# Optimization experiments

Hardware: AMD Instinct MI355X
Metric: run time of the kernel (lower is better)

## Reference

```python
import jax, jax.numpy as jnp
import numpy as np

B, H, T = 32, 80, 1600
C1, C2 = 32, 32
K, S, P = 3, 2, 1  # kernel, stride, padding on both dims


def setup_inputs() -> dict:
    key = jax.random.key(0)
    k1, k2, k3, k4, k5, k6 = jax.random.split(key, 6)
    inputs = jax.random.normal(k1, (B, 1, H, T), dtype=jnp.float32)
    seq_lengths = jax.random.randint(k2, (B,), 1, T + 1).astype(jnp.int32)
    W1 = jax.random.normal(k3, (C1, 1, K, K), dtype=jnp.float32) * 0.1
    b1 = jax.random.normal(k4, (C1,), dtype=jnp.float32) * 0.1
    W2 = jax.random.normal(k5, (C2, C1, K, K), dtype=jnp.float32) * 0.05
    b2 = jax.random.normal(k6, (C2,), dtype=jnp.float32) * 0.1
    return {"inputs": inputs, "seq_lengths": seq_lengths,
            "W1": W1, "b1": b1, "W2": W2, "b2": b2}


def _conv(x, W, b):
    y = jax.lax.conv_general_dilated(
        x, W, window_strides=(S, S), padding=((P, P), (P, P)),
        dimension_numbers=("NCHW", "OIHW", "NCHW"))
    return y + b[None, :, None, None]


def _new_lengths(L):
    # floor((L + 2p - d*(k-1) - 1)/s) + 1, matching _get_sequence_lengths
    return (L + 2 * P - (K - 1) - 1) // S + 1


def _mask_time(x, L):
    # zero positions t >= L[b] along the last (time) axis
    t = jnp.arange(x.shape[3])
    valid = (t[None, :] < L[:, None]).astype(x.dtype)  # [B, Tout]
    return x * valid[:, None, None, :]


def reference(inputs, seq_lengths, W1, b1, W2, b2):
    # conv1 + mask
    x = _conv(inputs, W1, b1)
    L = _new_lengths(seq_lengths)
    x = _mask_time(x, L)
    # relu + mask (lengths unchanged)
    x = _mask_time(jax.nn.relu(x), L)
    # conv2 + mask
    x = _conv(x, W2, b2)
    L = _new_lengths(L)
    x = _mask_time(x, L)
    # relu + mask
    x = _mask_time(jax.nn.relu(x), L)
    return x, L
```

## Files before the change

kernel.cpp:

```cpp
#include <hip/hip_runtime.h>
#include <hip/hip_bf16.h>

#define B_    32
#define H_IN  80
#define T_IN  1600
#define C1_   32
#define H1_   40
#define T1_   800
#define C2_   32
#define H2_   20
#define T2_   400

#define TH2   2
#define TT2   32
#define NH1   5
#define NT1   65
#define NIDX  33
#define RROWS 11
#define RCOLSW 66
#define RWORDS (RROWS * RCOLSW)

#define NPOS   (NH1 * NT1)
#define NCHUNK 11

#define WS_W2FRAGS 1152
#define WS_W1OFF   1152
#define WS_TOTAL   1216
#define OUTN  (B_ * C2_ * H2_ * T2_)

typedef unsigned int uint32;
typedef __attribute__((ext_vector_type(8)))  short short8;
typedef __attribute__((ext_vector_type(4)))  float f32x4;
typedef __attribute__((ext_vector_type(16))) float f32x16;
typedef __attribute__((ext_vector_type(2)))  uint32 u32x2;
typedef __attribute__((ext_vector_type(4)))  uint32 u32x4;

__device__ __forceinline__ unsigned short f2bf(float x) {
    __hip_bfloat16 h = __float2bfloat16(x);
    return __builtin_bit_cast(unsigned short, h);
}

__device__ __forceinline__ int x1off(int h1r, int t1r, int g) {
    int idx = t1r >> 1;
    int par = t1r & 1;
    return ((par * (NH1 * NIDX) + h1r * NIDX + idx) << 6) + (((g ^ idx) & 3) << 4);
}

__global__ void wprep(const float* __restrict__ W2, const float* __restrict__ W1,
                      const float* __restrict__ b1, unsigned short* __restrict__ ws) {
    int i = blockIdx.x * 256 + threadIdx.x;
    if (i < WS_W2FRAGS) {
        int mt   = i / 576;
        int rem  = i - mt * 576;
        int tap  = rem >> 6;
        int lane = rem & 63;
        int lg   = lane >> 4;
        int l15  = lane & 15;
        int c2   = mt * 16 + l15;
        short8 f;
#pragma unroll
        for (int j = 0; j < 8; ++j)
            f[j] = (short)f2bf(W2[((c2 * C1_) + lg * 8 + j) * 9 + tap]);
        *((short8*)ws + i) = f;
    } else if (i < WS_TOTAL) {
        int lane = i - WS_W1OFF;
        int c1 = lane & 31;
        int kb = (lane >> 5) * 8;
        short8 f;
#pragma unroll
        for (int j = 0; j < 8; ++j) {
            int k = kb + j;
            float v = (k < 9) ? W1[c1 * 9 + k] : (k == 9 ? b1[c1] : 0.0f);
            f[j] = (short)f2bf(v);
        }
        *((short8*)ws + i) = f;
    }
}

__global__ __launch_bounds__(256, 6) void fused_conv(
    const float* __restrict__ in, const int* __restrict__ seq,
    const float* __restrict__ b2,
    const unsigned short* __restrict__ ws,
    float* __restrict__ out)
{
    __shared__ __align__(16) char   x1mem[2 * NH1 * NIDX * 64];
    __shared__ __align__(16) uint32 raw32[RWORDS];

    const int tid  = threadIdx.x;
    const int lane = tid & 63;
    const int wv   = tid >> 6;
    const int l15  = lane & 15;
    const int lg   = lane >> 4;
    const int hi   = lane >> 5;
    const int n32  = lane & 31;
    const int b      = blockIdx.z;
    const int h2base = blockIdx.y * TH2;
    const int t2base = blockIdx.x * TT2;

    const int L  = seq[b];
    const int L1 = ((L  - 1) >> 1) + 1;
    const int L2 = ((L1 - 1) >> 1) + 1;

    if (blockIdx.x == 0 && blockIdx.y == 0 && tid == 0)
        out[OUTN + b] = (float)L2;

    if (t2base >= L2) {
#pragma unroll
        for (int k = 0; k < 8; ++k) {
            int i = tid + k * 256;
            int row = i >> 5, col = i & 31;
            int c2 = row >> 1, r = row & 1;
            int t2 = t2base + col;
            if (t2 < T2_)
                out[((b * C2_ + c2) * H2_ + h2base + r) * T2_ + t2] = 0.0f;
        }
        return;
    }

    const int row0 = 4 * h2base - 3;
    const int t0   = 4 * t2base - 3;
    const float* inb = in + b * (H_IN * T_IN);
#pragma unroll
    for (int k = 0; k < 3; ++k) {
        int pi = tid + k * 256;
        if (pi < RWORDS) {
            int row = pi / RCOLSW;
            int q   = pi - row * RCOLSW;
            int h = row0 + row;
            int t = t0 + 2 * q;
            bool hok = (h >= 0) & (h < H_IN);
            bool ok0 = hok & (t >= 0) & (t < T_IN);
            bool ok1 = hok & (t + 1 >= 0) & (t + 1 < T_IN);
            float v0 = inb[ok0 ? h * T_IN + t     : 0];
            float v1 = inb[ok1 ? h * T_IN + t + 1 : 0];
            v0 = ok0 ? v0 : 0.0f;
            v1 = ok1 ? v1 : 0.0f;
            raw32[pi] = (uint32)f2bf(v0) | ((uint32)f2bf(v1) << 16);
        }
    }

    const short8 w1f = *((const short8*)ws + WS_W1OFF + lane);
    const int mt    = wv & 1;
    const int strip = wv >> 1;
    short8 afr[9];
#pragma unroll
    for (int tap = 0; tap < 9; ++tap)
        afr[tap] = *((const short8*)ws + (mt * 9 + tap) * 64 + lane);
    float b2r[4];
#pragma unroll
    for (int j = 0; j < 4; ++j) b2r[j] = b2[mt * 16 + lg * 4 + j];

    __syncthreads();

    const int h1base = 2 * h2base - 1;
    const int t1base = 2 * t2base - 1;
    for (int c = wv; c < NCHUNK; c += 4) {
        int p  = c * 32 + n32;
        int pc = p < NPOS ? p : NPOS - 1;
        int h1r = pc / NT1;
        int t1r = pc - h1r * NT1;

        const uint32* rp = raw32 + (2 * h1r) * RCOLSW + t1r;
        uint32 a0 = rp[0],            b0v = rp[1];
        uint32 a1 = rp[RCOLSW],       b1v = rp[RCOLSW + 1];
        uint32 a2 = rp[2 * RCOLSW],   b2v = rp[2 * RCOLSW + 1];

        uint32 w0l = a0;
        uint32 w1l = (b0v & 0xffffu) | (a1 << 16);
        uint32 w2l = (a1 >> 16) | (b1v << 16);
        uint32 w3l = a2;
        uint32 w0h = (b2v & 0xffffu) | 0x3f800000u;

        uint32 fw0 = hi ? w0h : w0l;
        uint32 fw1 = hi ? 0u  : w1l;
        uint32 fw2 = hi ? 0u  : w2l;
        uint32 fw3 = hi ? 0u  : w3l;
        short8 bfrag = __builtin_bit_cast(short8, (u32x4){fw0, fw1, fw2, fw3});

        f32x16 acc = {};
        acc = __builtin_amdgcn_mfma_f32_32x32x16_bf16(w1f, bfrag, acc, 0, 0, 0);

        int h1 = h1base + h1r;
        int t1 = t1base + t1r;
        bool okp = (h1 >= 0) && (t1 >= 0) && (t1 < L1);
        if (p < NPOS) {
#pragma unroll
            for (int g = 0; g < 4; ++g) {
                float v0 = okp ? fmaxf(acc[4 * g + 0], 0.0f) : 0.0f;
                float v1 = okp ? fmaxf(acc[4 * g + 1], 0.0f) : 0.0f;
                float v2 = okp ? fmaxf(acc[4 * g + 2], 0.0f) : 0.0f;
                float v3 = okp ? fmaxf(acc[4 * g + 3], 0.0f) : 0.0f;
                u32x2 dw;
                dw.x = (uint32)f2bf(v0) | ((uint32)f2bf(v1) << 16);
                dw.y = (uint32)f2bf(v2) | ((uint32)f2bf(v3) << 16);
                *(u32x2*)(x1mem + x1off(h1r, t1r, g) + hi * 8) = dw;
            }
        }
    }

    __syncthreads();

    f32x4 acc2[TH2];
#pragma unroll
    for (int r = 0; r < TH2; ++r) acc2[r] = (f32x4){0.f, 0.f, 0.f, 0.f};

#pragma unroll
    for (int tap = 0; tap < 9; ++tap) {
        const int kh = tap / 3;
        const int kt = tap % 3;
        const int t1r = 2 * (strip * 16 + l15) + kt;
#pragma unroll
        for (int r = 0; r < TH2; ++r) {
            short8 bx = *(const short8*)(x1mem + x1off(2 * r + kh, t1r, lg));
            acc2[r] = __builtin_amdgcn_mfma_f32_16x16x32_bf16(afr[tap], bx, acc2[r], 0, 0, 0);
        }
    }

    __syncthreads();

    float* obuf = (float*)x1mem;
    {
        const int t2 = t2base + strip * 16 + l15;
        const bool vm = (t2 < L2);
#pragma unroll
        for (int r = 0; r < TH2; ++r) {
#pragma unroll
            for (int j = 0; j < 4; ++j) {
                int c2 = mt * 16 + lg * 4 + j;
                float v = acc2[r][j] + b2r[j];
                v = vm ? fmaxf(v, 0.0f) : 0.0f;
                obuf[(c2 * TH2 + r) * 33 + strip * 16 + l15] = v;
            }
        }
    }
    __syncthreads();

#pragma unroll
    for (int k = 0; k < 8; ++k) {
        int i = tid + k * 256;
        int row = i >> 5, col = i & 31;
        int c2 = row >> 1, r = row & 1;
        int t2 = t2base + col;
        if (t2 < T2_)
            out[((b * C2_ + c2) * H2_ + h2base + r) * T2_ + t2] = obuf[row * 33 + col];
    }
}

extern "C" void kernel_launch(void* const* d_in, const int* in_sizes, int n_in,
                              void* d_out, int out_size, void* d_ws, size_t ws_size,
                              hipStream_t stream) {
    const float* in  = (const float*)d_in[0];
    const int*   seq = (const int*)d_in[1];
    const float* W1  = (const float*)d_in[2];
    const float* b1  = (const float*)d_in[3];
    const float* W2  = (const float*)d_in[4];
    const float* b2  = (const float*)d_in[5];
    float* out = (float*)d_out;
    unsigned short* ws = (unsigned short*)d_ws;

    wprep<<<dim3((WS_TOTAL + 255) / 256), dim3(256), 0, stream>>>(W2, W1, b1, ws);

    dim3 grid((T2_ + TT2 - 1) / TT2, H2_ / TH2, B_);
    fused_conv<<<grid, dim3(256), 0, stream>>>(in, seq, b2, ws, out);
}
```

Before: 26.59 us.

## Double h2 tile height and switch conv2 to 32x32 MFMA with direct stores

Measured after the change: 26.97 us. No clear change (+1.4%).

```diff
diff --git a/kernel.cpp b/kernel.cpp
--- a/kernel.cpp
+++ b/kernel.cpp
@@ -11,17 +11,17 @@
 #define H2_   20
 #define T2_   400
 
-#define TH2   2
+#define TH2   4
 #define TT2   32
-#define NH1   5
+#define NH1   9
 #define NT1   65
 #define NIDX  33
-#define RROWS 11
+#define RROWS 19
 #define RCOLSW 66
 #define RWORDS (RROWS * RCOLSW)
 
 #define NPOS   (NH1 * NT1)
-#define NCHUNK 11
+#define NCHUNK 19
 
 #define WS_W2FRAGS 1152
 #define WS_W1OFF   1152
@@ -50,17 +50,16 @@
                       const float* __restrict__ b1, unsigned short* __restrict__ ws) {
     int i = blockIdx.x * 256 + threadIdx.x;
     if (i < WS_W2FRAGS) {
-        int mt   = i / 576;
-        int rem  = i - mt * 576;
-        int tap  = rem >> 6;
-        int lane = rem & 63;
-        int lg   = lane >> 4;
-        int l15  = lane & 15;
-        int c2   = mt * 16 + l15;
+        int th   = i >> 6;
+        int lane = i & 63;
+        int tap  = th >> 1;
+        int half = th & 1;
+        int c2   = lane & 31;
+        int hi   = lane >> 5;
         short8 f;
 #pragma unroll
         for (int j = 0; j < 8; ++j)
-            f[j] = (short)f2bf(W2[((c2 * C1_) + lg * 8 + j) * 9 + tap]);
+            f[j] = (short)f2bf(W2[(c2 * C1_ + half * 16 + hi * 8 + j) * 9 + tap]);
         *((short8*)ws + i) = f;
     } else if (i < WS_TOTAL) {
         int lane = i - WS_W1OFF;
@@ -77,7 +76,7 @@
     }
 }
 
-__global__ __launch_bounds__(256, 6) void fused_conv(
+__global__ __launch_bounds__(256, 3) void fused_conv(
     const float* __restrict__ in, const int* __restrict__ seq,
     const float* __restrict__ b2,
     const unsigned short* __restrict__ ws,
@@ -89,8 +88,6 @@
     const int tid  = threadIdx.x;
     const int lane = tid & 63;
     const int wv   = tid >> 6;
-    const int l15  = lane & 15;
-    const int lg   = lane >> 4;
     const int hi   = lane >> 5;
     const int n32  = lane & 31;
     const int b      = blockIdx.z;
@@ -105,14 +102,15 @@
         out[OUTN + b] = (float)L2;
 
     if (t2base >= L2) {
-#pragma unroll
-        for (int k = 0; k < 8; ++k) {
+        const f32x4 z4 = (f32x4){0.f, 0.f, 0.f, 0.f};
+#pragma unroll
+        for (int k = 0; k < 4; ++k) {
             int i = tid + k * 256;
-            int row = i >> 5, col = i & 31;
-            int c2 = row >> 1, r = row & 1;
-            int t2 = t2base + col;
-            if (t2 < T2_)
-                out[((b * C2_ + c2) * H2_ + h2base + r) * T2_ + t2] = 0.0f;
+            int row = i >> 3, colq = i & 7;
+            int c2 = row >> 2, r = row & 3;
+            int t2q = t2base + colq * 4;
+            if (t2q < T2_)
+                *(f32x4*)(out + ((b * C2_ + c2) * H2_ + h2base + r) * T2_ + t2q) = z4;
         }
         return;
     }
@@ -121,7 +119,7 @@
     const int t0   = 4 * t2base - 3;
     const float* inb = in + b * (H_IN * T_IN);
 #pragma unroll
-    for (int k = 0; k < 3; ++k) {
+    for (int k = 0; k < 5; ++k) {
         int pi = tid + k * 256;
         if (pi < RWORDS) {
             int row = pi / RCOLSW;
@@ -140,15 +138,12 @@
     }
 
     const short8 w1f = *((const short8*)ws + WS_W1OFF + lane);
-    const int mt    = wv & 1;
-    const int strip = wv >> 1;
-    short8 afr[9];
-#pragma unroll
-    for (int tap = 0; tap < 9; ++tap)
-        afr[tap] = *((const short8*)ws + (mt * 9 + tap) * 64 + lane);
-    float b2r[4];
-#pragma unroll
-    for (int j = 0; j < 4; ++j) b2r[j] = b2[mt * 16 + lg * 4 + j];
+    f32x4 b2v4[4];
+    {
+        const f32x4* b2p = (const f32x4*)b2;
+#pragma unroll
+        for (int q = 0; q < 4; ++q) b2v4[q] = b2p[2 * q + hi];
+    }
 
     __syncthreads();
 
@@ -200,49 +195,32 @@
 
     __syncthreads();
 
-    f32x4 acc2[TH2];
-#pragma unroll
-    for (int r = 0; r < TH2; ++r) acc2[r] = (f32x4){0.f, 0.f, 0.f, 0.f};
-
+    const int r = wv;
+    f32x16 acc = {};
 #pragma unroll
     for (int tap = 0; tap < 9; ++tap) {
         const int kh = tap / 3;
         const int kt = tap % 3;
-        const int t1r = 2 * (strip * 16 + l15) + kt;
-#pragma unroll
-        for (int r = 0; r < TH2; ++r) {
-            short8 bx = *(const short8*)(x1mem + x1off(2 * r + kh, t1r, lg));
-            acc2[r] = __builtin_amdgcn_mfma_f32_16x16x32_bf16(afr[tap], bx, acc2[r], 0, 0, 0);
-        }
-    }
-
-    __syncthreads();
-
-    float* obuf = (float*)x1mem;
-    {
-        const int t2 = t2base + strip * 16 + l15;
+        const int t1r = 2 * n32 + kt;
+#pragma unroll
+        for (int half = 0; half < 2; ++half) {
+            short8 a = *((const short8*)ws + (tap * 2 + half) * 64 + lane);
+            short8 bx = *(const short8*)(x1mem + x1off(2 * r + kh, t1r, half * 2 + hi));
+            acc = __builtin_amdgcn_mfma_f32_32x32x16_bf16(a, bx, acc, 0, 0, 0);
+        }
+    }
+
+    const int t2 = t2base + n32;
+    if (t2 < T2_) {
         const bool vm = (t2 < L2);
-#pragma unroll
-        for (int r = 0; r < TH2; ++r) {
-#pragma unroll
-            for (int j = 0; j < 4; ++j) {
-                int c2 = mt * 16 + lg * 4 + j;
-                float v = acc2[r][j] + b2r[j];
-                v = vm ? fmaxf(v, 0.0f) : 0.0f;
-                obuf[(c2 * TH2 + r) * 33 + strip * 16 + l15] = v;
-            }
-        }
-    }
-    __syncthreads();
-
-#pragma unroll
-    for (int k = 0; k < 8; ++k) {
-        int i = tid + k * 256;
-        int row = i >> 5, col = i & 31;
-        int c2 = row >> 1, r = row & 1;
-        int t2 = t2base + col;
-        if (t2 < T2_)
-            out[((b * C2_ + c2) * H2_ + h2base + r) * T2_ + t2] = obuf[row * 33 + col];
+        float* outb = out + ((b * C2_) * H2_ + h2base + r) * T2_ + t2;
+#pragma unroll
+        for (int reg = 0; reg < 16; ++reg) {
+            int c2 = (reg & 3) + 8 * (reg >> 2) + 4 * hi;
+            float v = acc[reg] + b2v4[reg >> 2][reg & 3];
+            v = vm ? fmaxf(v, 0.0f) : 0.0f;
+            outb[c2 * (H2_ * T2_)] = v;
+        }
     }
 }
 
```

## Convert fused conv to persistent blocks with register-prefetched input tiles

Applied to the files above, without the earlier changes.

Result: slower. 38.76 us (+45.8%).

```diff
diff --git a/kernel.cpp b/kernel.cpp
--- a/kernel.cpp
+++ b/kernel.cpp
@@ -23,6 +23,10 @@
 #define NPOS   (NH1 * NT1)
 #define NCHUNK 11
 
+#define NQ      130
+#define NBLK    1280
+#define QSTRIDE (NBLK / B_)
+
 #define WS_W2FRAGS 1152
 #define WS_W1OFF   1152
 #define WS_TOTAL   1216
@@ -44,6 +48,32 @@
     int idx = t1r >> 1;
     int par = t1r & 1;
     return ((par * (NH1 * NIDX) + h1r * NIDX + idx) << 6) + (((g ^ idx) & 3) << 4);
+}
+
+__device__ __forceinline__ void stage_load(const float* __restrict__ inb, int tid,
+                                           int h2base, int t2base, uint32 rv[3]) {
+    const int row0 = 4 * h2base - 3;
+    const int t0   = 4 * t2base - 3;
+#pragma unroll
+    for (int k = 0; k < 3; ++k) {
+        int pi = tid + k * 256;
+        uint32 v = 0u;
+        if (pi < RWORDS) {
+            int row = pi / RCOLSW;
+            int qd  = pi - row * RCOLSW;
+            int h = row0 + row;
+            int t = t0 + 2 * qd;
+            bool hok = (h >= 0) & (h < H_IN);
+            bool ok0 = hok & (t >= 0) & (t < T_IN);
+            bool ok1 = hok & (t + 1 >= 0) & (t + 1 < T_IN);
+            float v0 = inb[ok0 ? h * T_IN + t     : 0];
+            float v1 = inb[ok1 ? h * T_IN + t + 1 : 0];
+            v0 = ok0 ? v0 : 0.0f;
+            v1 = ok1 ? v1 : 0.0f;
+            v = (uint32)f2bf(v0) | ((uint32)f2bf(v1) << 16);
+        }
+        rv[k] = v;
+    }
 }
 
 __global__ void wprep(const float* __restrict__ W2, const float* __restrict__ W1,
@@ -77,7 +107,7 @@
     }
 }
 
-__global__ __launch_bounds__(256, 6) void fused_conv(
+__global__ __launch_bounds__(256, 5) void fused_conv(
     const float* __restrict__ in, const int* __restrict__ seq,
     const float* __restrict__ b2,
     const unsigned short* __restrict__ ws,
@@ -93,18 +123,155 @@
     const int lg   = lane >> 4;
     const int hi   = lane >> 5;
     const int n32  = lane & 31;
-    const int b      = blockIdx.z;
-    const int h2base = blockIdx.y * TH2;
-    const int t2base = blockIdx.x * TT2;
+
+    const int b  = blockIdx.x & (B_ - 1);
+    const int q0 = blockIdx.x >> 5;
 
     const int L  = seq[b];
     const int L1 = ((L  - 1) >> 1) + 1;
     const int L2 = ((L1 - 1) >> 1) + 1;
 
-    if (blockIdx.x == 0 && blockIdx.y == 0 && tid == 0)
+    if (q0 == 0 && tid == 0)
         out[OUTN + b] = (float)L2;
 
-    if (t2base >= L2) {
+    const short8 w1f = *((const short8*)ws + WS_W1OFF + lane);
+    const int mt    = wv & 1;
+    const int strip = wv >> 1;
+    short8 afr[9];
+#pragma unroll
+    for (int tap = 0; tap < 9; ++tap)
+        afr[tap] = *((const short8*)ws + (mt * 9 + tap) * 64 + lane);
+    float b2r[4];
+#pragma unroll
+    for (int j = 0; j < 4; ++j) b2r[j] = b2[mt * 16 + lg * 4 + j];
+
+    const float* inb = in + b * (H_IN * T_IN);
+
+    uint32 rv[3];
+    for (int q = q0; q < NQ; q += QSTRIDE) {
+        int t2i = q / 10;
+        if (t2i * TT2 < L2) {
+            stage_load(inb, tid, (q - t2i * 10) * TH2, t2i * TT2, rv);
+            break;
+        }
+    }
+
+    for (int q = q0; q < NQ; q += QSTRIDE) {
+        const int t2i = q / 10;
+        const int h2i = q - t2i * 10;
+        const int t2base = t2i * TT2;
+        const int h2base = h2i * TH2;
+
+        if (t2base >= L2) {
+            const f32x4 z4 = (f32x4){0.f, 0.f, 0.f, 0.f};
+#pragma unroll
+            for (int k = 0; k < 2; ++k) {
+                int i = tid + k * 256;
+                int row = i >> 3, colq = i & 7;
+                int c2 = row >> 1, r = row & 1;
+                int t2q = t2base + colq * 4;
+                if (t2q < T2_)
+                    *(f32x4*)(out + ((b * C2_ + c2) * H2_ + h2base + r) * T2_ + t2q) = z4;
+            }
+            continue;
+        }
+
+#pragma unroll
+        for (int k = 0; k < 3; ++k) {
+            int pi = tid + k * 256;
+            if (pi < RWORDS) raw32[pi] = rv[k];
+        }
+        __syncthreads();
+
+        const int h1base = 2 * h2base - 1;
+        const int t1base = 2 * t2base - 1;
+        for (int c = wv; c < NCHUNK; c += 4) {
+            int p  = c * 32 + n32;
+            int pc = p < NPOS ? p : NPOS - 1;
+            int h1r = pc / NT1;
+            int t1r = pc - h1r * NT1;
+
+            const uint32* rp = raw32 + (2 * h1r) * RCOLSW + t1r;
+            uint32 a0 = rp[0],            b0v = rp[1];
+            uint32 a1 = rp[RCOLSW],       b1v = rp[RCOLSW + 1];
+            uint32 a2 = rp[2 * RCOLSW],   b2v = rp[2 * RCOLSW + 1];
+
+            uint32 w0l = a0;
+            uint32 w1l = (b0v & 0xffffu) | (a1 << 16);
+            uint32 w2l = (a1 >> 16) | (b1v << 16);
+            uint32 w3l = a2;
+            uint32 w0h = (b2v & 0xffffu) | 0x3f800000u;
+
+            uint32 fw0 = hi ? w0h : w0l;
+            uint32 fw1 = hi ? 0u  : w1l;
+            uint32 fw2 = hi ? 0u  : w2l;
+            uint32 fw3 = hi ? 0u  : w3l;
+            short8 bfrag = __builtin_bit_cast(short8, (u32x4){fw0, fw1, fw2, fw3});
+
+            f32x16 acc = {};
+            acc = __builtin_amdgcn_mfma_f32_32x32x16_bf16(w1f, bfrag, acc, 0, 0, 0);
+
+            int h1 = h1base + h1r;
+            int t1 = t1base + t1r;
+            bool okp = (h1 >= 0) && (t1 >= 0) && (t1 < L1);
+            if (p < NPOS) {
+#pragma unroll
+                for (int g = 0; g < 4; ++g) {
+                    float v0 = okp ? fmaxf(acc[4 * g + 0], 0.0f) : 0.0f;
+                    float v1 = okp ? fmaxf(acc[4 * g + 1], 0.0f) : 0.0f;
+                    float v2 = okp ? fmaxf(acc[4 * g + 2], 0.0f) : 0.0f;
+                    float v3 = okp ? fmaxf(acc[4 * g + 3], 0.0f) : 0.0f;
+                    u32x2 dw;
+                    dw.x = (uint32)f2bf(v0) | ((uint32)f2bf(v1) << 16);
+                    dw.y = (uint32)f2bf(v2) | ((uint32)f2bf(v3) << 16);
+                    *(u32x2*)(x1mem + x1off(h1r, t1r, g) + hi * 8) = dw;
+                }
+            }
+        }
+        __syncthreads();
+
+        for (int q2 = q + QSTRIDE; q2 < NQ; q2 += QSTRIDE) {
+            int tt = q2 / 10;
+            if (tt * TT2 < L2) {
+                stage_load(inb, tid, (q2 - tt * 10) * TH2, tt * TT2, rv);
+                break;
+            }
+        }
+
+        f32x4 acc2[TH2];
+#pragma unroll
+        for (int r = 0; r < TH2; ++r) acc2[r] = (f32x4){0.f, 0.f, 0.f, 0.f};
+
+#pragma unroll
+        for (int tap = 0; tap < 9; ++tap) {
+            const int kh = tap / 3;
+            const int kt = tap % 3;
+            const int t1r = 2 * (strip * 16 + l15) + kt;
+#pragma unroll
+            for (int r = 0; r < TH2; ++r) {
+                short8 bx = *(const short8*)(x1mem + x1off(2 * r + kh, t1r, lg));
+                acc2[r] = __builtin_amdgcn_mfma_f32_16x16x32_bf16(afr[tap], bx, acc2[r], 0, 0, 0);
+            }
+        }
+        __syncthreads();
+
+        float* obuf = (float*)x1mem;
+        {
+            const int t2 = t2base + strip * 16 + l15;
+            const bool vm = (t2 < L2);
+#pragma unroll
+            for (int r = 0; r < TH2; ++r) {
+#pragma unroll
+                for (int j = 0; j < 4; ++j) {
+                    int c2 = mt * 16 + lg * 4 + j;
+                    float v = acc2[r][j] + b2r[j];
+                    v = vm ? fmaxf(v, 0.0f) : 0.0f;
+                    obuf[(c2 * TH2 + r) * 33 + strip * 16 + l15] = v;
+                }
+            }
+        }
+        __syncthreads();
+
 #pragma unroll
         for (int k = 0; k < 8; ++k) {
             int i = tid + k * 256;
@@ -112,137 +279,8 @@
             int c2 = row >> 1, r = row & 1;
             int t2 = t2base + col;
             if (t2 < T2_)
-                out[((b * C2_ + c2) * H2_ + h2base + r) * T2_ + t2] = 0.0f;
-        }
-        return;
-    }
-
-    const int row0 = 4 * h2base - 3;
-    const int t0   = 4 * t2base - 3;
-    const float* inb = in + b * (H_IN * T_IN);
-#pragma unroll
-    for (int k = 0; k < 3; ++k) {
-        int pi = tid + k * 256;
-        if (pi < RWORDS) {
-            int row = pi / RCOLSW;
-            int q   = pi - row * RCOLSW;
-            int h = row0 + row;
-            int t = t0 + 2 * q;
-            bool hok = (h >= 0) & (h < H_IN);
-            bool ok0 = hok & (t >= 0) & (t < T_IN);
-            bool ok1 = hok & (t + 1 >= 0) & (t + 1 < T_IN);
-            float v0 = inb[ok0 ? h * T_IN + t     : 0];
-            float v1 = inb[ok1 ? h * T_IN + t + 1 : 0];
-            v0 = ok0 ? v0 : 0.0f;
-            v1 = ok1 ? v1 : 0.0f;
-            raw32[pi] = (uint32)f2bf(v0) | ((uint32)f2bf(v1) << 16);
-        }
-    }
-
-    const short8 w1f = *((const short8*)ws + WS_W1OFF + lane);
-    const int mt    = wv & 1;
-    const int strip = wv >> 1;
-    short8 afr[9];
-#pragma unroll
-    for (int tap = 0; tap < 9; ++tap)
-        afr[tap] = *((const short8*)ws + (mt * 9 + tap) * 64 + lane);
-    float b2r[4];
-#pragma unroll
-    for (int j = 0; j < 4; ++j) b2r[j] = b2[mt * 16 + lg * 4 + j];
-
-    __syncthreads();
-
-    const int h1base = 2 * h2base - 1;
-    const int t1base = 2 * t2base - 1;
-    for (int c = wv; c < NCHUNK; c += 4) {
-        int p  = c * 32 + n32;
-        int pc = p < NPOS ? p : NPOS - 1;
-        int h1r = pc / NT1;
-        int t1r = pc - h1r * NT1;
-
-        const uint32* rp = raw32 + (2 * h1r) * RCOLSW + t1r;
-        uint32 a0 = rp[0],            b0v = rp[1];
-        uint32 a1 = rp[RCOLSW],       b1v = rp[RCOLSW + 1];
-        uint32 a2 = rp[2 * RCOLSW],   b2v = rp[2 * RCOLSW + 1];
-
-        uint32 w0l = a0;
-        uint32 w1l = (b0v & 0xffffu) | (a1 << 16);
-        uint32 w2l = (a1 >> 16) | (b1v << 16);
-        uint32 w3l = a2;
-        uint32 w0h = (b2v & 0xffffu) | 0x3f800000u;
-
-        uint32 fw0 = hi ? w0h : w0l;
-        uint32 fw1 = hi ? 0u  : w1l;
-        uint32 fw2 = hi ? 0u  : w2l;
-        uint32 fw3 = hi ? 0u  : w3l;
-        short8 bfrag = __builtin_bit_cast(short8, (u32x4){fw0, fw1, fw2, fw3});
-
-        f32x16 acc = {};
-        acc = __builtin_amdgcn_mfma_f32_32x32x16_bf16(w1f, bfrag, acc, 0, 0, 0);
-
-        int h1 = h1base + h1r;
-        int t1 = t1base + t1r;
-        bool okp = (h1 >= 0) && (t1 >= 0) && (t1 < L1);
-        if (p < NPOS) {
-#pragma unroll
-            for (int g = 0; g < 4; ++g) {
-                float v0 = okp ? fmaxf(acc[4 * g + 0], 0.0f) : 0.0f;
-                float v1 = okp ? fmaxf(acc[4 * g + 1], 0.0f) : 0.0f;
-                float v2 = okp ? fmaxf(acc[4 * g + 2], 0.0f) : 0.0f;
-                float v3 = okp ? fmaxf(acc[4 * g + 3], 0.0f) : 0.0f;
-                u32x2 dw;
-                dw.x = (uint32)f2bf(v0) | ((uint32)f2bf(v1) << 16);
-                dw.y = (uint32)f2bf(v2) | ((uint32)f2bf(v3) << 16);
-                *(u32x2*)(x1mem + x1off(h1r, t1r, g) + hi * 8) = dw;
-            }
-        }
-    }
-
-    __syncthreads();
-
-    f32x4 acc2[TH2];
-#pragma unroll
-    for (int r = 0; r < TH2; ++r) acc2[r] = (f32x4){0.f, 0.f, 0.f, 0.f};
-
-#pragma unroll
-    for (int tap = 0; tap < 9; ++tap) {
-        const int kh = tap / 3;
-        const int kt = tap % 3;
-        const int t1r = 2 * (strip * 16 + l15) + kt;
-#pragma unroll
-        for (int r = 0; r < TH2; ++r) {
-            short8 bx = *(const short8*)(x1mem + x1off(2 * r + kh, t1r, lg));
-            acc2[r] = __builtin_amdgcn_mfma_f32_16x16x32_bf16(afr[tap], bx, acc2[r], 0, 0, 0);
-        }
-    }
-
-    __syncthreads();
-
-    float* obuf = (float*)x1mem;
-    {
-        const int t2 = t2base + strip * 16 + l15;
-        const bool vm = (t2 < L2);
-#pragma unroll
-        for (int r = 0; r < TH2; ++r) {
-#pragma unroll
-            for (int j = 0; j < 4; ++j) {
-                int c2 = mt * 16 + lg * 4 + j;
-                float v = acc2[r][j] + b2r[j];
-                v = vm ? fmaxf(v, 0.0f) : 0.0f;
-                obuf[(c2 * TH2 + r) * 33 + strip * 16 + l15] = v;
-            }
-        }
-    }
-    __syncthreads();
-
-#pragma unroll
-    for (int k = 0; k < 8; ++k) {
-        int i = tid + k * 256;
-        int row = i >> 5, col = i & 31;
-        int c2 = row >> 1, r = row & 1;
-        int t2 = t2base + col;
-        if (t2 < T2_)
-            out[((b * C2_ + c2) * H2_ + h2base + r) * T2_ + t2] = obuf[row * 33 + col];
+                out[((b * C2_ + c2) * H2_ + h2base + r) * T2_ + t2] = obuf[row * 33 + col];
+        }
     }
 }
 
@@ -260,6 +298,5 @@
 
     wprep<<<dim3((WS_TOTAL + 255) / 256), dim3(256), 0, stream>>>(W2, W1, b1, ws);
 
-    dim3 grid((T2_ + TT2 - 1) / TT2, H2_ / TH2, B_);
-    fused_conv<<<grid, dim3(256), 0, stream>>>(in, seq, b2, ws, out);
-}
+    fused_conv<<<dim3(NBLK), dim3(256), 0, stream>>>(in, seq, b2, ws, out);
+}
```

## Give each wave an independent 1x16 output tile with private LDS

Applied to the files above, without the earlier changes.

Result: slower. 28.05 us (+5.5%).

```diff
diff --git a/kernel.cpp b/kernel.cpp
--- a/kernel.cpp
+++ b/kernel.cpp
@@ -11,22 +11,16 @@
 #define H2_   20
 #define T2_   400
 
-#define TH2   2
-#define TT2   32
-#define NH1   5
-#define NT1   65
-#define NIDX  33
-#define RROWS 11
-#define RCOLSW 66
-#define RWORDS (RROWS * RCOLSW)
-
-#define NPOS   (NH1 * NT1)
-#define NCHUNK 11
+#define WSTRIDE 7584
+#define RAWOFF  6528
+#define RCW     34
+#define RWTOT   238
+#define NPOSW   99
+#define OUTN  (B_ * C2_ * H2_ * T2_)
 
 #define WS_W2FRAGS 1152
 #define WS_W1OFF   1152
 #define WS_TOTAL   1216
-#define OUTN  (B_ * C2_ * H2_ * T2_)
 
 typedef unsigned int uint32;
 typedef __attribute__((ext_vector_type(8)))  short short8;
@@ -43,7 +37,7 @@
 __device__ __forceinline__ int x1off(int h1r, int t1r, int g) {
     int idx = t1r >> 1;
     int par = t1r & 1;
-    return ((par * (NH1 * NIDX) + h1r * NIDX + idx) << 6) + (((g ^ idx) & 3) << 4);
+    return ((par * 51 + h1r * 17 + idx) << 6) + (((g ^ idx) & 3) << 4);
 }
 
 __global__ void wprep(const float* __restrict__ W2, const float* __restrict__ W1,
@@ -77,14 +71,13 @@
     }
 }
 
-__global__ __launch_bounds__(256, 6) void fused_conv(
+__global__ __launch_bounds__(256, 5) void fused_conv(
     const float* __restrict__ in, const int* __restrict__ seq,
     const float* __restrict__ b2,
     const unsigned short* __restrict__ ws,
     float* __restrict__ out)
 {
-    __shared__ __align__(16) char   x1mem[2 * NH1 * NIDX * 64];
-    __shared__ __align__(16) uint32 raw32[RWORDS];
+    __shared__ __align__(16) char lds[4 * WSTRIDE];
 
     const int tid  = threadIdx.x;
     const int lane = tid & 63;
@@ -93,156 +86,154 @@
     const int lg   = lane >> 4;
     const int hi   = lane >> 5;
     const int n32  = lane & 31;
-    const int b      = blockIdx.z;
-    const int h2base = blockIdx.y * TH2;
-    const int t2base = blockIdx.x * TT2;
+    const int b    = blockIdx.z;
+    const int h2   = blockIdx.y;
+    const int t2q  = blockIdx.x;
 
     const int L  = seq[b];
     const int L1 = ((L  - 1) >> 1) + 1;
     const int L2 = ((L1 - 1) >> 1) + 1;
 
-    if (blockIdx.x == 0 && blockIdx.y == 0 && tid == 0)
+    if (t2q == 0 && h2 == 0 && tid == 0)
         out[OUTN + b] = (float)L2;
 
-    if (t2base >= L2) {
-#pragma unroll
-        for (int k = 0; k < 8; ++k) {
+    if (64 * t2q >= L2) {
+        const f32x4 z4 = (f32x4){0.f, 0.f, 0.f, 0.f};
+#pragma unroll
+        for (int k = 0; k < 2; ++k) {
             int i = tid + k * 256;
-            int row = i >> 5, col = i & 31;
-            int c2 = row >> 1, r = row & 1;
-            int t2 = t2base + col;
-            if (t2 < T2_)
-                out[((b * C2_ + c2) * H2_ + h2base + r) * T2_ + t2] = 0.0f;
+            int c2 = i >> 4, q = i & 15;
+            int t2g = 64 * t2q + 4 * q;
+            if (t2g < T2_)
+                *(f32x4*)(out + ((b * C2_ + c2) * H2_ + h2) * T2_ + t2g) = z4;
         }
         return;
     }
 
-    const int row0 = 4 * h2base - 3;
-    const int t0   = 4 * t2base - 3;
-    const float* inb = in + b * (H_IN * T_IN);
-#pragma unroll
-    for (int k = 0; k < 3; ++k) {
-        int pi = tid + k * 256;
-        if (pi < RWORDS) {
-            int row = pi / RCOLSW;
-            int q   = pi - row * RCOLSW;
-            int h = row0 + row;
-            int t = t0 + 2 * q;
-            bool hok = (h >= 0) & (h < H_IN);
-            bool ok0 = hok & (t >= 0) & (t < T_IN);
-            bool ok1 = hok & (t + 1 >= 0) & (t + 1 < T_IN);
-            float v0 = inb[ok0 ? h * T_IN + t     : 0];
-            float v1 = inb[ok1 ? h * T_IN + t + 1 : 0];
-            v0 = ok0 ? v0 : 0.0f;
-            v1 = ok1 ? v1 : 0.0f;
-            raw32[pi] = (uint32)f2bf(v0) | ((uint32)f2bf(v1) << 16);
-        }
-    }
+    char*   myl = lds + wv * WSTRIDE;
+    uint32* raw = (uint32*)(myl + RAWOFF);
+    const int t2i    = t2q * 4 + wv;
+    const int t2base = t2i * 16;
+    const bool wave_zero = (t2base >= L2);
 
     const short8 w1f = *((const short8*)ws + WS_W1OFF + lane);
-    const int mt    = wv & 1;
-    const int strip = wv >> 1;
-    short8 afr[9];
-#pragma unroll
-    for (int tap = 0; tap < 9; ++tap)
-        afr[tap] = *((const short8*)ws + (mt * 9 + tap) * 64 + lane);
-    float b2r[4];
-#pragma unroll
-    for (int j = 0; j < 4; ++j) b2r[j] = b2[mt * 16 + lg * 4 + j];
-
-    __syncthreads();
-
-    const int h1base = 2 * h2base - 1;
-    const int t1base = 2 * t2base - 1;
-    for (int c = wv; c < NCHUNK; c += 4) {
-        int p  = c * 32 + n32;
-        int pc = p < NPOS ? p : NPOS - 1;
-        int h1r = pc / NT1;
-        int t1r = pc - h1r * NT1;
-
-        const uint32* rp = raw32 + (2 * h1r) * RCOLSW + t1r;
-        uint32 a0 = rp[0],            b0v = rp[1];
-        uint32 a1 = rp[RCOLSW],       b1v = rp[RCOLSW + 1];
-        uint32 a2 = rp[2 * RCOLSW],   b2v = rp[2 * RCOLSW + 1];
-
-        uint32 w0l = a0;
-        uint32 w1l = (b0v & 0xffffu) | (a1 << 16);
-        uint32 w2l = (a1 >> 16) | (b1v << 16);
-        uint32 w3l = a2;
-        uint32 w0h = (b2v & 0xffffu) | 0x3f800000u;
-
-        uint32 fw0 = hi ? w0h : w0l;
-        uint32 fw1 = hi ? 0u  : w1l;
-        uint32 fw2 = hi ? 0u  : w2l;
-        uint32 fw3 = hi ? 0u  : w3l;
-        short8 bfrag = __builtin_bit_cast(short8, (u32x4){fw0, fw1, fw2, fw3});
-
-        f32x16 acc = {};
-        acc = __builtin_amdgcn_mfma_f32_32x32x16_bf16(w1f, bfrag, acc, 0, 0, 0);
-
-        int h1 = h1base + h1r;
-        int t1 = t1base + t1r;
-        bool okp = (h1 >= 0) && (t1 >= 0) && (t1 < L1);
-        if (p < NPOS) {
-#pragma unroll
-            for (int g = 0; g < 4; ++g) {
-                float v0 = okp ? fmaxf(acc[4 * g + 0], 0.0f) : 0.0f;
-                float v1 = okp ? fmaxf(acc[4 * g + 1], 0.0f) : 0.0f;
-                float v2 = okp ? fmaxf(acc[4 * g + 2], 0.0f) : 0.0f;
-                float v3 = okp ? fmaxf(acc[4 * g + 3], 0.0f) : 0.0f;
-                u32x2 dw;
-                dw.x = (uint32)f2bf(v0) | ((uint32)f2bf(v1) << 16);
-                dw.y = (uint32)f2bf(v2) | ((uint32)f2bf(v3) << 16);
-                *(u32x2*)(x1mem + x1off(h1r, t1r, g) + hi * 8) = dw;
+
+    if (!wave_zero) {
+        const int row0 = 4 * h2 - 3;
+        const int t0   = 64 * t2i - 3;
+        const float* inb = in + b * (H_IN * T_IN);
+#pragma unroll
+        for (int k = 0; k < 4; ++k) {
+            int idx = lane + 64 * k;
+            if (idx < RWTOT) {
+                int row = idx / RCW;
+                int q   = idx - row * RCW;
+                int h = row0 + row;
+                int t = t0 + 2 * q;
+                bool hok = (h >= 0) & (h < H_IN);
+                bool ok0 = hok & (t >= 0) & (t < T_IN);
+                bool ok1 = hok & (t + 1 >= 0) & (t + 1 < T_IN);
+                float v0 = inb[ok0 ? h * T_IN + t     : 0];
+                float v1 = inb[ok1 ? h * T_IN + t + 1 : 0];
+                v0 = ok0 ? v0 : 0.0f;
+                v1 = ok1 ? v1 : 0.0f;
+                raw[row * RCW + q] = (uint32)f2bf(v0) | ((uint32)f2bf(v1) << 16);
             }
         }
-    }
-
-    __syncthreads();
-
-    f32x4 acc2[TH2];
-#pragma unroll
-    for (int r = 0; r < TH2; ++r) acc2[r] = (f32x4){0.f, 0.f, 0.f, 0.f};
-
-#pragma unroll
-    for (int tap = 0; tap < 9; ++tap) {
-        const int kh = tap / 3;
-        const int kt = tap % 3;
-        const int t1r = 2 * (strip * 16 + l15) + kt;
-#pragma unroll
-        for (int r = 0; r < TH2; ++r) {
-            short8 bx = *(const short8*)(x1mem + x1off(2 * r + kh, t1r, lg));
-            acc2[r] = __builtin_amdgcn_mfma_f32_16x16x32_bf16(afr[tap], bx, acc2[r], 0, 0, 0);
-        }
-    }
-
-    __syncthreads();
-
-    float* obuf = (float*)x1mem;
-    {
-        const int t2 = t2base + strip * 16 + l15;
+
+#pragma unroll
+        for (int c = 0; c < 4; ++c) {
+            int p  = c * 32 + n32;
+            int pc = p < NPOSW ? p : NPOSW - 1;
+            int h1r = pc / 33;
+            int t1r = pc - 33 * h1r;
+
+            const uint32* rp = raw + (2 * h1r) * RCW + t1r;
+            uint32 r0a = rp[0],           r0b = rp[1];
+            uint32 r1a = rp[RCW],         r1b = rp[RCW + 1];
+            uint32 r2a = rp[2 * RCW],     r2b = rp[2 * RCW + 1];
+
+            uint32 w0l = r0a;
+            uint32 w1l = (r0b & 0xffffu) | (r1a << 16);
+            uint32 w2l = (r1a >> 16) | (r1b << 16);
+            uint32 w3l = r2a;
+            uint32 w0h = (r2b & 0xffffu) | 0x3f800000u;
+
+            uint32 fw0 = hi ? w0h : w0l;
+            uint32 fw1 = hi ? 0u  : w1l;
+            uint32 fw2 = hi ? 0u  : w2l;
+            uint32 fw3 = hi ? 0u  : w3l;
+            short8 bfrag = __builtin_bit_cast(short8, (u32x4){fw0, fw1, fw2, fw3});
+
+            f32x16 acc = {};
+            acc = __builtin_amdgcn_mfma_f32_32x32x16_bf16(w1f, bfrag, acc, 0, 0, 0);
+
+            int h1 = 2 * h2 - 1 + h1r;
+            int t1 = 32 * t2i - 1 + t1r;
+            bool okp = (h1 >= 0) && (t1 >= 0) && (t1 < L1);
+            if (p < NPOSW) {
+#pragma unroll
+                for (int g = 0; g < 4; ++g) {
+                    float v0 = okp ? fmaxf(acc[4 * g + 0], 0.0f) : 0.0f;
+                    float v1 = okp ? fmaxf(acc[4 * g + 1], 0.0f) : 0.0f;
+                    float v2 = okp ? fmaxf(acc[4 * g + 2], 0.0f) : 0.0f;
+                    float v3 = okp ? fmaxf(acc[4 * g + 3], 0.0f) : 0.0f;
+                    u32x2 dw;
+                    dw.x = (uint32)f2bf(v0) | ((uint32)f2bf(v1) << 16);
+                    dw.y = (uint32)f2bf(v2) | ((uint32)f2bf(v3) << 16);
+                    *(u32x2*)(myl + x1off(h1r, t1r, g) + hi * 8) = dw;
+                }
+            }
+        }
+
+        f32x4 acc2[2];
+        acc2[0] = (f32x4){0.f, 0.f, 0.f, 0.f};
+        acc2[1] = (f32x4){0.f, 0.f, 0.f, 0.f};
+#pragma unroll
+        for (int tap = 0; tap < 9; ++tap) {
+            const int kh = tap / 3;
+            const int kt = tap % 3;
+            const int t1r = 2 * l15 + kt;
+            short8 bx  = *(const short8*)(myl + x1off(kh, t1r, lg));
+            short8 af0 = *((const short8*)ws + tap * 64 + lane);
+            short8 af1 = *((const short8*)ws + (9 + tap) * 64 + lane);
+            acc2[0] = __builtin_amdgcn_mfma_f32_16x16x32_bf16(af0, bx, acc2[0], 0, 0, 0);
+            acc2[1] = __builtin_amdgcn_mfma_f32_16x16x32_bf16(af1, bx, acc2[1], 0, 0, 0);
+        }
+
+        float* obuf = (float*)myl;
+        const int t2 = t2base + l15;
         const bool vm = (t2 < L2);
-#pragma unroll
-        for (int r = 0; r < TH2; ++r) {
+        const f32x4* b2p = (const f32x4*)b2;
+#pragma unroll
+        for (int mt = 0; mt < 2; ++mt) {
+            f32x4 bb = b2p[mt * 4 + lg];
 #pragma unroll
             for (int j = 0; j < 4; ++j) {
                 int c2 = mt * 16 + lg * 4 + j;
-                float v = acc2[r][j] + b2r[j];
+                float v = acc2[mt][j] + bb[j];
                 v = vm ? fmaxf(v, 0.0f) : 0.0f;
-                obuf[(c2 * TH2 + r) * 33 + strip * 16 + l15] = v;
+                obuf[c2 * 16 + l15] = v;
             }
         }
-    }
+    } else {
+        u32x2* ob = (u32x2*)myl;
+        const u32x2 z = (u32x2){0u, 0u};
+#pragma unroll
+        for (int k = 0; k < 4; ++k) ob[lane + 64 * k] = z;
+    }
+
     __syncthreads();
 
 #pragma unroll
     for (int k = 0; k < 8; ++k) {
         int i = tid + k * 256;
-        int row = i >> 5, col = i & 31;
-        int c2 = row >> 1, r = row & 1;
-        int t2 = t2base + col;
-        if (t2 < T2_)
-            out[((b * C2_ + c2) * H2_ + h2base + r) * T2_ + t2] = obuf[row * 33 + col];
+        int c2 = i >> 6, col = i & 63;
+        int wsel = col >> 4;
+        int t2g = 64 * t2q + col;
+        float f = *(const float*)(lds + wsel * WSTRIDE + (c2 * 16 + (col & 15)) * 4);
+        if (t2g < T2_)
+            out[((b * C2_ + c2) * H2_ + h2) * T2_ + t2g] = f;
     }
 }
 
@@ -260,6 +251,6 @@
 
     wprep<<<dim3((WS_TOTAL + 255) / 256), dim3(256), 0, stream>>>(W2, W1, b1, ws);
 
-    dim3 grid((T2_ + TT2 - 1) / TT2, H2_ / TH2, B_);
+    dim3 grid(7, H2_, B_);
     fused_conv<<<grid, dim3(256), 0, stream>>>(in, seq, b2, ws, out);
 }
```
